# Kernel optimization log

Measured on AMD Instinct MI355X. Metric: run time of the kernel, lower is better.

Reference implementation:

```python
import jax, jax.numpy as jnp
import numpy as np

B, CIN, COUT, H, W = 4, 256, 256, 64, 64
EPS = 1e-5


def _conv1x1(x, w, b):
    # x: [B,C,H,W], w: [O,C], b: [O]
    return jnp.einsum('bchw,oc->bohw', x, w) + b[:, None, None]


def _conv3x3(x, w, b):
    y = jax.lax.conv_general_dilated(x, w, (1, 1), 'SAME',
                                     dimension_numbers=('NCHW', 'OIHW', 'NCHW'))
    return y + b[:, None, None]


def _bn(x, g, b, m, v):
    # inference-mode BatchNorm2d
    return g[:, None, None] * (x - m[:, None, None]) * jax.lax.rsqrt(v[:, None, None] + EPS) + b[:, None, None]


def setup_inputs():
    key = jax.random.key(0)
    keys = iter(jax.random.split(key, 64))
    nrm = lambda shape, s=0.05: jax.random.normal(next(keys), shape, dtype=jnp.float32) * s
    uni = lambda shape: jax.random.uniform(next(keys), shape, dtype=jnp.float32, minval=0.5, maxval=1.5)
    C, C2 = COUT, COUT // 2
    d = {}
    d['x'] = nrm((B, CIN, H, W), 1.0)
    d['wq'] = nrm((C2, CIN)); d['bq'] = nrm((C2,))
    d['wk'] = nrm((C2, CIN)); d['bk'] = nrm((C2,))
    d['wv'] = nrm((C, CIN)); d['bv'] = nrm((C,))
    d['d1_w'] = nrm((C, C)); d['d1_b'] = nrm((C,))
    for p in ['bn1', 'lbn1', 'lbn2', 'lbn3']:
        d[p + '_g'] = uni((C,)); d[p + '_b'] = nrm((C,))
        d[p + '_m'] = nrm((C,)); d[p + '_v'] = uni((C,))
    d['l1_w'] = nrm((C, C)); d['l1_b'] = nrm((C,))
    d['l2_w'] = nrm((C, C, 3, 3)); d['l2_b'] = nrm((C,))
    d['l3_w'] = nrm((C, C)); d['l3_b'] = nrm((C,))
    d['r1_w'] = nrm((C2, C)); d['r1_b'] = nrm((C2,))
    d['rbn_g'] = uni((C2,)); d['rbn_b'] = nrm((C2,))
    d['rbn_m'] = nrm((C2,)); d['rbn_v'] = uni((C2,))
    d['r2_w'] = nrm((C, C2)); d['r2_b'] = nrm((C,))
    return d


def _forward(x, wq, bq, wk, bk, wv, bv, d1_w, d1_b,
             bn1_g, bn1_b, bn1_m, bn1_v,
             l1_w, l1_b, lbn1_g, lbn1_b, lbn1_m, lbn1_v,
             l2_w, l2_b, lbn2_g, lbn2_b, lbn2_m, lbn2_v,
             l3_w, l3_b, lbn3_g, lbn3_b, lbn3_m, lbn3_v,
             r1_w, r1_b, rbn_g, rbn_b, rbn_m, rbn_v, r2_w, r2_b):
    b, _, h, w = x.shape
    n = h * w
    q = _conv1x1(x, wq, bq).reshape(b, -1, n)   # [B, C/2, N]
    k = _conv1x1(x, wk, bk).reshape(b, -1, n)   # [B, C/2, N]
    v = _conv1x1(x, wv, bv).reshape(b, -1, n)   # [B, C,   N]
    energy = jnp.einsum('bcn,bcm->bnm', q, k)   # [B, N, N] (query^T key)
    attn = jax.nn.softmax(energy, axis=-1)
    # feature = bmm(value, attn^T): feat[b,c,n] = sum_m v[b,c,m] * attn[b,n,m]
    feat = jnp.einsum('bcm,bnm->bcn', v, attn).reshape(b, -1, h, w)
    # dual1 gate: sigmoid(relu(bn(conv1x1(feat))))
    gate1 = jax.nn.sigmoid(jax.nn.relu(_bn(_conv1x1(feat, d1_w, d1_b), bn1_g, bn1_b, bn1_m, bn1_v)))
    y = feat * gate1
    # dual2_l: 1x1 -> 3x3 -> 1x1 conv/bn/relu stack
    yl = jax.nn.relu(_bn(_conv1x1(y, l1_w, l1_b), lbn1_g, lbn1_b, lbn1_m, lbn1_v))
    yl = jax.nn.relu(_bn(_conv3x3(yl, l2_w, l2_b), lbn2_g, lbn2_b, lbn2_m, lbn2_v))
    yl = jax.nn.relu(_bn(_conv1x1(yl, l3_w, l3_b), lbn3_g, lbn3_b, lbn3_m, lbn3_v))
    # dual2_r: global-avg-pool SE branch
    pooled = jnp.mean(y, axis=(2, 3), keepdims=True)  # [B, C, 1, 1]
    yr = jax.nn.relu(_bn(_conv1x1(pooled, r1_w, r1_b), rbn_g, rbn_b, rbn_m, rbn_v))
    yr = _conv1x1(yr, r2_w, r2_b)
    return feat * jax.nn.sigmoid(yl + yr)


def reference(x, wq, bq, wk, bk, wv, bv, d1_w, d1_b,
              bn1_g, bn1_b, bn1_m, bn1_v,
              l1_w, l1_b, lbn1_g, lbn1_b, lbn1_m, lbn1_v,
              l2_w, l2_b, lbn2_g, lbn2_b, lbn2_m, lbn2_v,
              l3_w, l3_b, lbn3_g, lbn3_b, lbn3_m, lbn3_v,
              r1_w, r1_b, rbn_g, rbn_b, rbn_m, rbn_v, r2_w, r2_b):
    return _forward(x, wq, bq, wk, bk, wv, bv, d1_w, d1_b,
                    bn1_g, bn1_b, bn1_m, bn1_v,
                    l1_w, l1_b, lbn1_g, lbn1_b, lbn1_m, lbn1_v,
                    l2_w, l2_b, lbn2_g, lbn2_b, lbn2_m, lbn2_v,
                    l3_w, l3_b, lbn3_g, lbn3_b, lbn3_m, lbn3_v,
                    r1_w, r1_b, rbn_g, rbn_b, rbn_m, rbn_v, r2_w, r2_b)
```

## Files before the change

kernel.cpp:

```cpp
#include <hip/hip_runtime.h>
#include <math.h>

#define NPIX 4096
#define EPSBN 1e-5f

typedef __attribute__((ext_vector_type(8))) short bf16x8;
typedef __attribute__((ext_vector_type(4))) float f32x4;

__device__ __forceinline__ float sigmoidf_(float x) { return 1.0f / (1.0f + expf(-x)); }

__device__ __forceinline__ short f2bf(float f) {
    unsigned u = __float_as_uint(f);
    u += 0x7fffu + ((u >> 16) & 1u);
    return (short)(u >> 16);
}
__device__ __forceinline__ float bf2f(short s) {
    return __uint_as_float(((unsigned)(unsigned short)s) << 16);
}
__device__ __forceinline__ int pk2(float lo, float hi) {
    return (int)(unsigned short)f2bf(lo) | ((int)(unsigned short)f2bf(hi) << 16);
}

__device__ __forceinline__ void gl_lds16(const short* g, short* l) {
    __builtin_amdgcn_global_load_lds(
        (const __attribute__((address_space(1))) void*)g,
        (__attribute__((address_space(3))) void*)l, 16, 0, 0);
}

template <int EPI, int BM, int BN>
__global__ __launch_bounds__(256) void gbt_k(
    const short* __restrict__ A, int lda,
    const short* __restrict__ B, int ldb,
    void* __restrict__ Cv, void* __restrict__ Cv2, int Ktot,
    const float* __restrict__ bias, const float* __restrict__ bias2,
    const float* __restrict__ bng, const float* __restrict__ bnb,
    const float* __restrict__ bnm, const float* __restrict__ bnv,
    const short* __restrict__ aux, const float* __restrict__ yrp)
{
    constexpr int FI = BM / 32, FJ = BN / 32;
    constexpr int SA = BM / 64, SB = BN / 64;
    __shared__ alignas(16) short lsA[2 * BM * 32];
    __shared__ alignas(16) short lsB[2 * BN * 32];

    const int tid = threadIdx.x;
    const int l = tid & 63;
    const int wv = tid >> 6;
    const int wm = wv >> 1, wn = wv & 1;
    const int m0 = blockIdx.y * BM;
    const int n0 = blockIdx.x * BN;

    const short* arow[2];
    const short* brow[2];
#pragma unroll
    for (int s = 0; s < SA; ++s) {
        int r = wv * (16 * SA) + s * 16 + (l >> 2);
        int sd = (l & 3) ^ ((r >> 1) & 3);
        if (EPI == 5) {
            int g = m0 + r;
            int p = (g >> 12) * 4356 + (((g & 4095) >> 6) + 1) * 66 + ((g & 63) + 1);
            arow[s] = A + (size_t)p * 256 + (sd << 3);
        } else {
            arow[s] = A + (size_t)(m0 + r) * lda + (sd << 3);
        }
    }
#pragma unroll
    for (int s = 0; s < SB; ++s) {
        int r = wv * (16 * SB) + s * 16 + (l >> 2);
        int sd = (l & 3) ^ ((r >> 1) & 3);
        brow[s] = B + (size_t)(n0 + r) * ldb + (sd << 3);
    }

    const int ks = l >> 4;
    const int lc = l & 15;
    int aoff[FI], boff[FJ];
#pragma unroll
    for (int f = 0; f < FI; ++f) {
        int ra = wm * (BM / 2) + f * 16 + lc;
        aoff[f] = ra * 64 + ((ks ^ ((ra >> 1) & 3)) << 4);
    }
#pragma unroll
    for (int f = 0; f < FJ; ++f) {
        int rb = wn * (BN / 2) + f * 16 + lc;
        boff[f] = rb * 64 + ((ks ^ ((rb >> 1) & 3)) << 4);
    }

    auto stage = [&](int d, int k0l) {
        int eA, eB;
        if (EPI == 5) {
            int t = k0l >> 8, ci0 = k0l & 255;
            eA = ((t / 3) * 66 + (t % 3) - 67) * 256 + ci0;
            eB = t * 65536 + ci0;
        } else {
            eA = k0l; eB = k0l;
        }
        short* dA = lsA + d * (BM * 32) + wv * (SA * 512);
        short* dB = lsB + d * (BN * 32) + wv * (SB * 512);
#pragma unroll
        for (int s = 0; s < SA; ++s) gl_lds16(arow[s] + eA, dA + s * 512);
#pragma unroll
        for (int s = 0; s < SB; ++s) gl_lds16(brow[s] + eB, dB + s * 512);
    };

    f32x4 acc[FI][FJ] = {};
    const int nt = Ktot >> 5;

    stage(0, 0);
    __syncthreads();
    int cur = 0;
    for (int t = 0; t < nt; ++t) {
        if (t + 1 < nt) stage(cur ^ 1, (t + 1) << 5);
        bf16x8 af[FI], bfr[FJ];
#pragma unroll
        for (int f = 0; f < FI; ++f)
            af[f] = *(const bf16x8*)((const char*)lsA + cur * (BM * 64) + aoff[f]);
#pragma unroll
        for (int f = 0; f < FJ; ++f)
            bfr[f] = *(const bf16x8*)((const char*)lsB + cur * (BN * 64) + boff[f]);
#pragma unroll
        for (int i = 0; i < FI; ++i)
#pragma unroll
            for (int j = 0; j < FJ; ++j)
                acc[i][j] = __builtin_amdgcn_mfma_f32_16x16x32_bf16(af[i], bfr[j], acc[i][j], 0, 0, 0);
        __syncthreads();
        cur ^= 1;
    }

    const int lr = (l >> 4) << 2;
#pragma unroll
    for (int i = 0; i < FI; ++i) {
        const int rowl = wm * (BM / 2) + i * 16 + lr;
#pragma unroll
        for (int j = 0; j < FJ; ++j) {
            const int coll = n0 + wn * (BN / 2) + j * 16 + lc;

            float sc = 0.f, tc = 0.f, bi = 0.f;
            if constexpr (EPI == 1) {
                bi = (coll < 128) ? bias[coll] : bias2[coll - 128];
            } else if constexpr (EPI == 3 || EPI == 4 || EPI == 5) {
                sc = bng[coll] * rsqrtf(bnv[coll] + EPSBN);
                tc = bnb[coll] - bnm[coll] * sc;
                bi = bias[coll];
            }

#pragma unroll
            for (int r = 0; r < 4; ++r) {
                const int row = m0 + rowl + r;
                float vvv = acc[i][j][r];
                if constexpr (EPI == 1) {
                    float val = vvv + bi;
                    short hi = f2bf(val);
                    short lo = f2bf(val - bf2f(hi));
                    size_t rb = (size_t)row * 256;
                    if (coll < 128) {
                        short* qb_ = (short*)Cv;
                        qb_[rb + coll] = hi;
                        qb_[rb + 128 + coll] = lo;
                    } else {
                        short* kb_ = (short*)Cv2;
                        int c = coll - 128;
                        kb_[rb + c] = hi;
                        kb_[rb + 128 + c] = lo;
                    }
                } else if constexpr (EPI == 2) {
                    int bb = coll >> 12;
                    ((short*)Cv)[((size_t)bb * 256 + row) * 4096 + (coll & 4095)] = f2bf(vvv + bias[row]);
                } else if constexpr (EPI == 3) {
                    float g = sigmoidf_(fmaxf(sc * (vvv + bi) + tc, 0.f));
                    float fv = bf2f(aux[(size_t)row * 256 + coll]);
                    ((short*)Cv)[(size_t)row * 256 + coll] = f2bf(fv * g);
                } else if constexpr (EPI == 4) {
                    float rv = fmaxf(sc * (vvv + bi) + tc, 0.f);
                    int bb = row >> 12, n = row & 4095;
                    int pr = bb * 4356 + ((n >> 6) + 1) * 66 + (n & 63) + 1;
                    ((short*)Cv)[(size_t)pr * 256 + coll] = f2bf(rv);
                } else if constexpr (EPI == 5) {
                    float rv = fmaxf(sc * (vvv + bi) + tc, 0.f);
                    ((short*)Cv)[(size_t)row * 256 + coll] = f2bf(rv);
                } else if constexpr (EPI == 6) {
                    float s6 = bng[row] * rsqrtf(bnv[row] + EPSBN);
                    float t6 = bnb[row] - bnm[row] * s6;
                    int bb = coll >> 12;
                    float yl = fmaxf(s6 * (vvv + bias[row]) + t6, 0.f);
                    float sg = sigmoidf_(yl + yrp[bb * 256 + row]);
                    float fv = bf2f(aux[(size_t)coll * 256 + row]);
                    ((float*)Cv)[((size_t)bb * 256 + row) * 4096 + (coll & 4095)] = fv * sg;
                }
            }
        }
    }
}

__global__ __launch_bounds__(512, 2) void flash_k(
    const short* __restrict__ Q, const short* __restrict__ K,
    const short* __restrict__ V, short* __restrict__ Op, float* __restrict__ lp)
{
    __shared__ alignas(16) short smem[32768];

    const int tid = threadIdx.x;
    const int l = tid & 63;
    const int wv = tid >> 6;
    const int bid = blockIdx.x;
    const int combo = bid & 15;
    const int batch = combo >> 2;
    const int kvq = combo & 3;
    const int q0 = (bid >> 4) * 256;
    const int kv0 = kvq * 1024;

    const short* Qb = Q + (size_t)batch * 4096 * 256;
    const short* Kb = K + (size_t)batch * 4096 * 256;
    const short* Vb = V + (size_t)batch * 256 * 4096;

    const int lc = l & 15, ks = l >> 4;

    bf16x8 bq[2][8];
#pragma unroll
    for (int f = 0; f < 2; ++f)
#pragma unroll
        for (int cc = 0; cc < 8; ++cc)
            bq[f][cc] = *(const bf16x8*)(Qb +
                (size_t)(q0 + wv * 32 + f * 16 + lc) * 256 + cc * 32 + ks * 8);

    const short* ksrc[2]; short* kdst[2];
    const short* vsrc[2]; short* vdst[2];
#pragma unroll
    for (int i = 0; i < 2; ++i) {
        int row = wv * 4 + i * 2 + (l >> 5);
        int s = l & 31;
        int g = s ^ (row & 7);
        ksrc[i] = Kb + (size_t)(kv0 + row) * 256 + g * 8;
        kdst[i] = smem + wv * 1024 + i * 512;
        int c = wv * 32 + i * 16 + (l >> 2);
        int sv = l & 3;
        int gv = sv ^ ((c >> 1) & 3);
        vsrc[i] = Vb + (size_t)c * 4096 + kv0 + gv * 8;
        vdst[i] = smem + 16384 + wv * 1024 + i * 512;
    }
    auto stageKV = [&](int buf, int t) {
#pragma unroll
        for (int i = 0; i < 2; ++i) gl_lds16(ksrc[i] + (size_t)t * 8192, kdst[i] + buf * 8192);
#pragma unroll
        for (int i = 0; i < 2; ++i) gl_lds16(vsrc[i] + t * 32, vdst[i] + buf * 8192);
    };

    stageKV(0, 0);
    __syncthreads();

    const int kro = lc * 512;
    const int kxr = lc & 7;
    const int vb0 = lc * 64 + ((ks ^ ((lc >> 1) & 3)) << 4);
    const int addrA = (((ks & 1) * 2) * 16 + lc) * 4;
    const int addrB = addrA + 64;

    bf16x8 ones;
#pragma unroll
    for (int e = 0; e < 8; ++e) ones[e] = (short)0x3F80;

    f32x4 acc_o[2][16] = {};
    f32x4 acc_l[2] = {};

    int cur = 0;
    for (int t = 0; t < 32; ++t) {
        if (t + 1 < 32) stageKV(cur ^ 1, t + 1);

        const char* kb_ = (const char*)smem + cur * 16384;
        f32x4 s00 = {}, s01 = {}, s10 = {}, s11 = {};
        __builtin_amdgcn_s_setprio(1);
#pragma unroll
        for (int jc = 0; jc < 4; ++jc) {
#pragma unroll
            for (int kvf = 0; kvf < 2; ++kvf) {
                const char* rb_ = kb_ + kro + kvf * 8192;
                bf16x8 kh_ = *(const bf16x8*)(rb_ + ((((jc * 4) + ks) ^ kxr) << 4));
                bf16x8 kl_ = *(const bf16x8*)(rb_ + (((((jc + 4) * 4) + ks) ^ kxr) << 4));
                f32x4& sA = kvf ? s01 : s00;
                f32x4& sB = kvf ? s11 : s10;
                sA = __builtin_amdgcn_mfma_f32_16x16x32_bf16(kh_, bq[0][jc], sA, 0, 0, 0);
                sB = __builtin_amdgcn_mfma_f32_16x16x32_bf16(kh_, bq[1][jc], sB, 0, 0, 0);
                sA = __builtin_amdgcn_mfma_f32_16x16x32_bf16(kl_, bq[0][jc], sA, 0, 0, 0);
                sB = __builtin_amdgcn_mfma_f32_16x16x32_bf16(kl_, bq[1][jc], sB, 0, 0, 0);
                sA = __builtin_amdgcn_mfma_f32_16x16x32_bf16(kh_, bq[0][jc + 4], sA, 0, 0, 0);
                sB = __builtin_amdgcn_mfma_f32_16x16x32_bf16(kh_, bq[1][jc + 4], sB, 0, 0, 0);
            }
        }
        __builtin_amdgcn_s_setprio(0);

        bf16x8 pa[2];
#pragma unroll
        for (int f = 0; f < 2; ++f) {
            const f32x4& sa = f ? s10 : s00;
            const f32x4& sb = f ? s11 : s01;
            int u0 = pk2(__expf(sa[0]), __expf(sa[1]));
            int u1 = pk2(__expf(sa[2]), __expf(sa[3]));
            int u2 = pk2(__expf(sb[0]), __expf(sb[1]));
            int u3 = pk2(__expf(sb[2]), __expf(sb[3]));
            int a0 = __builtin_amdgcn_ds_bpermute(addrA, u0);
            int b0 = __builtin_amdgcn_ds_bpermute(addrA, u2);
            int a1 = __builtin_amdgcn_ds_bpermute(addrA, u1);
            int b1 = __builtin_amdgcn_ds_bpermute(addrA, u3);
            int a2 = __builtin_amdgcn_ds_bpermute(addrB, u0);
            int b2 = __builtin_amdgcn_ds_bpermute(addrB, u2);
            int a3 = __builtin_amdgcn_ds_bpermute(addrB, u1);
            int b3 = __builtin_amdgcn_ds_bpermute(addrB, u3);
            union { int i4[4]; bf16x8 v; } un;
            un.i4[0] = (ks < 2) ? a0 : b0;
            un.i4[1] = (ks < 2) ? a1 : b1;
            un.i4[2] = (ks < 2) ? a2 : b2;
            un.i4[3] = (ks < 2) ? a3 : b3;
            pa[f] = un.v;
        }

        const char* vbb = (const char*)smem + 32768 + cur * 16384;
        __builtin_amdgcn_s_setprio(1);
#pragma unroll
        for (int j = 0; j < 16; ++j) {
            bf16x8 vv = *(const bf16x8*)(vbb + vb0 + j * 1024);
            acc_o[0][j] = __builtin_amdgcn_mfma_f32_16x16x32_bf16(pa[0], vv, acc_o[0][j], 0, 0, 0);
            acc_o[1][j] = __builtin_amdgcn_mfma_f32_16x16x32_bf16(pa[1], vv, acc_o[1][j], 0, 0, 0);
        }
        acc_l[0] = __builtin_amdgcn_mfma_f32_16x16x32_bf16(pa[0], ones, acc_l[0], 0, 0, 0);
        acc_l[1] = __builtin_amdgcn_mfma_f32_16x16x32_bf16(pa[1], ones, acc_l[1], 0, 0, 0);
        __builtin_amdgcn_s_setprio(0);
        __syncthreads();
        cur ^= 1;
    }

    short* Ob = Op + ((size_t)combo * 4096 + q0 + wv * 32) * 256;
#pragma unroll
    for (int f = 0; f < 2; ++f)
#pragma unroll
        for (int j = 0; j < 16; ++j)
#pragma unroll
            for (int r = 0; r < 4; ++r)
                Ob[(size_t)(f * 16 + ks * 4 + r) * 256 + j * 16 + lc] = f2bf(acc_o[f][j][r]);
    if (lc == 0) {
        float* lb = lp + (size_t)combo * 4096 + q0 + wv * 32;
#pragma unroll
        for (int f = 0; f < 2; ++f)
#pragma unroll
            for (int r = 0; r < 4; ++r)
                lb[f * 16 + ks * 4 + r] = acc_l[f][r];
    }
}

__global__ __launch_bounds__(256) void combine_k(const short* __restrict__ Op,
                                                 const float* __restrict__ lp,
                                                 short* __restrict__ o)
{
    int idx = blockIdx.x * 256 + threadIdx.x;
    size_t e = (size_t)idx * 4;
    int row = (int)(e >> 8);
    int batch = row >> 12, ql = row & 4095;
    int c = (int)(e & 255);
    size_t lbase = (size_t)batch * 4 * 4096 + ql;
    float li = 1.0f / (lp[lbase] + lp[lbase + 4096] + lp[lbase + 8192] + lp[lbase + 12288]);
    size_t base = ((size_t)(batch * 4) * 4096 + ql) * 256 + c;
    const short4 a = *(const short4*)(Op + base);
    const short4 b = *(const short4*)(Op + base + 1048576);
    const short4 cc = *(const short4*)(Op + base + 2097152);
    const short4 d = *(const short4*)(Op + base + 3145728);
    short4 o4;
    o4.x = f2bf((bf2f(a.x) + bf2f(b.x) + bf2f(cc.x) + bf2f(d.x)) * li);
    o4.y = f2bf((bf2f(a.y) + bf2f(b.y) + bf2f(cc.y) + bf2f(d.y)) * li);
    o4.z = f2bf((bf2f(a.z) + bf2f(b.z) + bf2f(cc.z) + bf2f(d.z)) * li);
    o4.w = f2bf((bf2f(a.w) + bf2f(b.w) + bf2f(cc.w) + bf2f(d.w)) * li);
    *(short4*)(o + (size_t)row * 256 + c) = o4;
}

__global__ __launch_bounds__(256) void transpose_x_k(const float* __restrict__ x,
                                                     short* __restrict__ xT3)
{
    __shared__ float t[64][65];
    const int b = blockIdx.z, c0 = blockIdx.y * 64, n0 = blockIdx.x * 64;
    const int tid = threadIdx.x;
#pragma unroll
    for (int rep = 0; rep < 16; ++rep) {
        int idx = tid + rep * 256;
        int i = idx >> 6, j = idx & 63;
        t[i][j] = x[((size_t)(b * 256 + c0 + i)) * NPIX + n0 + j];
    }
    __syncthreads();
#pragma unroll
    for (int rep = 0; rep < 16; ++rep) {
        int idx = tid + rep * 256;
        int i = idx >> 6, j = idx & 63;
        float v = t[j][i];
        short hi = f2bf(v);
        short lo = f2bf(v - bf2f(hi));
        size_t rb = ((size_t)(b * NPIX + n0 + i)) * 768;
        xT3[rb + c0 + j] = hi;
        xT3[rb + 256 + c0 + j] = hi;
        xT3[rb + 512 + c0 + j] = lo;
    }
}

__global__ __launch_bounds__(256) void prep_k(
    const float* __restrict__ wq, const float* __restrict__ wk,
    const float* __restrict__ wvp, const float* __restrict__ d1w,
    const float* __restrict__ l1w, const float* __restrict__ l3w,
    const float* __restrict__ l2w,
    short* __restrict__ wqk3, short* __restrict__ wvb, short* __restrict__ d1wb,
    short* __restrict__ l1wb, short* __restrict__ l3wb, short* __restrict__ w2b)
{
    const int b = blockIdx.x;
    const int tid = threadIdx.x;
    if (b < 256) {
        int idx = b * 256 + tid;
        int o = idx >> 8, c = idx & 255;
        const float* src = (o < 128) ? wq : wk;
        float v = src[(o & 127) * 256 + c];
        short hi = f2bf(v);
        short lo = f2bf(v - bf2f(hi));
        size_t rb = (size_t)o * 768;
        wqk3[rb + c] = hi;
        wqk3[rb + 256 + c] = lo;
        wqk3[rb + 512 + c] = hi;
    } else if (b < 1280) {
        int g = (b - 256) >> 8;
        int i = ((b - 256) & 255) * 256 + tid;
        const float* s = g == 0 ? wvp : g == 1 ? d1w : g == 2 ? l1w : l3w;
        short* d = g == 0 ? wvb : g == 1 ? d1wb : g == 2 ? l1wb : l3wb;
        d[i] = f2bf(s[i]);
    } else {
        int idx = (b - 1280) * 256 + tid;
        int t = idx >> 16;
        int rem = idx & 65535;
        int co = rem >> 8, ci = rem & 255;
        w2b[idx] = f2bf(l2w[((size_t)(co * 256 + ci)) * 9 + t]);
    }
}

__global__ __launch_bounds__(256) void pool_s1_k(const short* __restrict__ yT,
                                                 float* __restrict__ ppart)
{
    const int ns = blockIdx.x, cg = blockIdx.y, b = blockIdx.z;
    const int tid = threadIdx.x;
    const int cl = tid & 63, ph = tid >> 6;
    float s = 0.f;
    const int nbase = ns * 256;
    for (int n = ph; n < 256; n += 4)
        s += bf2f(yT[((size_t)(b * NPIX + nbase + n)) * 256 + cg * 64 + cl]);
    __shared__ float ls[4][64];
    ls[ph][cl] = s;
    __syncthreads();
    if (ph == 0)
        ppart[((size_t)(b * 4 + cg) * 16 + ns) * 64 + cl] =
            ls[0][cl] + ls[1][cl] + ls[2][cl] + ls[3][cl];
}

__global__ __launch_bounds__(256) void pool_s2_k(const float* __restrict__ ppart,
                                                 float* __restrict__ pooled)
{
    const int b = blockIdx.x;
    const int c = threadIdx.x;
    const int cg = c >> 6, cl = c & 63;
    float s = 0.f;
#pragma unroll
    for (int ns = 0; ns < 16; ++ns)
        s += ppart[((size_t)(b * 4 + cg) * 16 + ns) * 64 + cl];
    pooled[b * 256 + c] = s * (1.0f / NPIX);
}

__global__ __launch_bounds__(256) void se_k(
    const float* __restrict__ pooled,
    const float* __restrict__ r1w, const float* __restrict__ r1b,
    const float* __restrict__ g, const float* __restrict__ bb,
    const float* __restrict__ m, const float* __restrict__ vv,
    const float* __restrict__ r2w, const float* __restrict__ r2b,
    float* __restrict__ yr)
{
    const int b = blockIdx.x;
    const int tid = threadIdx.x;
    __shared__ float p[256], hbuf[128];
    p[tid] = pooled[b * 256 + tid];
    __syncthreads();
    if (tid < 128) {
        float a = r1b[tid];
        for (int ci = 0; ci < 256; ++ci) a = fmaf(r1w[tid * 256 + ci], p[ci], a);
        float s = g[tid] * rsqrtf(vv[tid] + EPSBN);
        float t = bb[tid] - m[tid] * s;
        hbuf[tid] = fmaxf(s * a + t, 0.f);
    }
    __syncthreads();
    float a = r2b[tid];
    for (int c2 = 0; c2 < 128; ++c2) a = fmaf(r2w[tid * 128 + c2], hbuf[c2], a);
    yr[b * 256 + tid] = a;
}

extern "C" void kernel_launch(void* const* d_in, const int* in_sizes, int n_in,
                              void* d_out, int out_size, void* d_ws, size_t ws_size,
                              hipStream_t stream)
{
    const float* x    = (const float*)d_in[0];
    const float* wq   = (const float*)d_in[1];
    const float* bq   = (const float*)d_in[2];
    const float* wk   = (const float*)d_in[3];
    const float* bk   = (const float*)d_in[4];
    const float* wvp  = (const float*)d_in[5];
    const float* bv   = (const float*)d_in[6];
    const float* d1w  = (const float*)d_in[7];
    const float* d1b  = (const float*)d_in[8];
    const float* bn1g = (const float*)d_in[9];
    const float* bn1b = (const float*)d_in[10];
    const float* bn1m = (const float*)d_in[11];
    const float* bn1v = (const float*)d_in[12];
    const float* lbn1g = (const float*)d_in[13];
    const float* lbn1b = (const float*)d_in[14];
    const float* lbn1m = (const float*)d_in[15];
    const float* lbn1v = (const float*)d_in[16];
    const float* lbn2g = (const float*)d_in[17];
    const float* lbn2b = (const float*)d_in[18];
    const float* lbn2m = (const float*)d_in[19];
    const float* lbn2v = (const float*)d_in[20];
    const float* lbn3g = (const float*)d_in[21];
    const float* lbn3b = (const float*)d_in[22];
    const float* lbn3m = (const float*)d_in[23];
    const float* lbn3v = (const float*)d_in[24];
    const float* l1w  = (const float*)d_in[25];
    const float* l1b  = (const float*)d_in[26];
    const float* l2w  = (const float*)d_in[27];
    const float* l2b  = (const float*)d_in[28];
    const float* l3w  = (const float*)d_in[29];
    const float* l3b  = (const float*)d_in[30];
    const float* r1w  = (const float*)d_in[31];
    const float* r1b  = (const float*)d_in[32];
    const float* rbng = (const float*)d_in[33];
    const float* rbnb = (const float*)d_in[34];
    const float* rbnm = (const float*)d_in[35];
    const float* rbnv = (const float*)d_in[36];
    const float* r2w  = (const float*)d_in[37];
    const float* r2b  = (const float*)d_in[38];

    float* out = (float*)d_out;
    char* wsb = (char*)d_ws;

    short* xT3  = (short*)(wsb);
    short* qbuf = (short*)(wsb + (24ull << 20));
    short* kbuf = (short*)(wsb + (32ull << 20));
    short* vbuf = (short*)(wsb + (40ull << 20));
    short* Opart= (short*)(wsb + (48ull << 20));
    short* featT= (short*)(wsb + (112ull << 20));
    float* lpart= (float*)(wsb + (120ull << 20));
    short* yT   = (short*)(wsb + (48ull << 20));
    short* t1pad= (short*)(wsb + (56ull << 20));
    short* t2T  = (short*)(wsb + (65ull << 20));
    short* wqk3 = (short*)(wsb + (121ull << 20));
    short* wvb  = wqk3 + 196608;
    short* d1wb = wvb + 65536;
    short* l1wb = d1wb + 65536;
    short* l3wb = l1wb + 65536;
    short* w2b  = l3wb + 65536;
    float* pooled = (float*)(wsb + (123ull << 20) + (512ull << 10));
    float* yrb  = pooled + 1024;
    float* ppart= yrb + 1024;

    dim3 blk(256);

    transpose_x_k<<<dim3(64, 4, 4), blk, 0, stream>>>(x, xT3);
    prep_k<<<3584, blk, 0, stream>>>(wq, wk, wvp, d1w, l1w, l3w, l2w,
                                     wqk3, wvb, d1wb, l1wb, l3wb, w2b);

    gbt_k<1, 128, 64><<<dim3(4, 128), blk, 0, stream>>>(xT3, 768, wqk3, 768, qbuf, kbuf, 768,
        bq, bk, nullptr, nullptr, nullptr, nullptr, nullptr, nullptr);
    gbt_k<2, 64, 128><<<dim3(128, 4), blk, 0, stream>>>(wvb, 256, xT3, 768, vbuf, nullptr, 256,
        bv, nullptr, nullptr, nullptr, nullptr, nullptr, nullptr, nullptr);

    flash_k<<<256, dim3(512), 0, stream>>>(qbuf, kbuf, vbuf, Opart, lpart);
    combine_k<<<4096, blk, 0, stream>>>(Opart, lpart, featT);

    gbt_k<3, 128, 64><<<dim3(4, 128), blk, 0, stream>>>(featT, 256, d1wb, 256, yT, nullptr, 256,
        d1b, nullptr, bn1g, bn1b, bn1m, bn1v, featT, nullptr);

    hipMemsetAsync(t1pad, 0, (size_t)4 * 4356 * 256 * 2, stream);

    pool_s1_k<<<dim3(16, 4, 4), blk, 0, stream>>>(yT, ppart);
    pool_s2_k<<<4, blk, 0, stream>>>(ppart, pooled);
    se_k<<<4, blk, 0, stream>>>(pooled, r1w, r1b, rbng, rbnb, rbnm, rbnv, r2w, r2b, yrb);

    gbt_k<4, 128, 64><<<dim3(4, 128), blk, 0, stream>>>(yT, 256, l1wb, 256, t1pad, nullptr, 256,
        l1b, nullptr, lbn1g, lbn1b, lbn1m, lbn1v, nullptr, nullptr);
    gbt_k<5, 128, 64><<<dim3(4, 128), blk, 0, stream>>>(t1pad, 256, w2b, 256, t2T, nullptr, 2304,
        l2b, nullptr, lbn2g, lbn2b, lbn2m, lbn2v, nullptr, nullptr);

    gbt_k<6, 64, 128><<<dim3(128, 4), blk, 0, stream>>>(l3wb, 256, t2T, 256, out, nullptr, 256,
        l3b, nullptr, lbn3g, lbn3b, lbn3m, lbn3v, featT, yrb);
}
```

Before: 250.5 us.

## Fuse pooling into gate GEMM, shrink split x buffer, drop bpermute in flash

Three separate changes. The channel-sum for global average pooling is now fused into the EPI==3 GEMM epilogue, which writes per-block partial sums, so the pool_s1 pass that re-read yT is removed. The x hi/lo split buffer shrinks from three copies to two, and the QK GEMM reuses the hi half through an index remap, which cuts the transpose write traffic. In flash attention, K rows are loaded into LDS in a permuted order, so the exp'd probabilities can be packed straight into the MFMA operand without ds_bpermute shuffles. The risk is correctness of the row permutation and the extra __syncthreads in the epilogue.

```diff
diff --git a/kernel.cpp b/kernel.cpp
--- a/kernel.cpp
+++ b/kernel.cpp
@@ -90,6 +90,9 @@
             int t = k0l >> 8, ci0 = k0l & 255;
             eA = ((t / 3) * 66 + (t % 3) - 67) * 256 + ci0;
             eB = t * 65536 + ci0;
+        } else if (EPI == 1) {
+            eA = (k0l < 256) ? k0l : k0l - 256;
+            eB = k0l;
         } else {
             eA = k0l; eB = k0l;
         }
@@ -125,6 +128,7 @@
         cur ^= 1;
     }
 
+    float colsum[FJ < 1 ? 1 : FJ] = {};
     const int lr = (l >> 4) << 2;
 #pragma unroll
     for (int i = 0; i < FI; ++i) {
@@ -167,7 +171,9 @@
                 } else if constexpr (EPI == 3) {
                     float g = sigmoidf_(fmaxf(sc * (vvv + bi) + tc, 0.f));
                     float fv = bf2f(aux[(size_t)row * 256 + coll]);
-                    ((short*)Cv)[(size_t)row * 256 + coll] = f2bf(fv * g);
+                    float yv = fv * g;
+                    ((short*)Cv)[(size_t)row * 256 + coll] = f2bf(yv);
+                    colsum[j] += yv;
                 } else if constexpr (EPI == 4) {
                     float rv = fmaxf(sc * (vvv + bi) + tc, 0.f);
                     int bb = row >> 12, n = row & 4095;
@@ -188,6 +194,22 @@
             }
         }
     }
+
+    if constexpr (EPI == 3) {
+        float* lsum = (float*)lsA;
+#pragma unroll
+        for (int j = 0; j < FJ; ++j) {
+            int cl = wn * (BN / 2) + j * 16 + lc;
+            lsum[cl * 8 + wm * 4 + ks] = colsum[j];
+        }
+        __syncthreads();
+        if (tid < BN) {
+            float s = 0.f;
+#pragma unroll
+            for (int u = 0; u < 8; ++u) s += lsum[tid * 8 + u];
+            ((float*)Cv2)[(size_t)blockIdx.y * 256 + n0 + tid] = s;
+        }
+    }
 }
 
 __global__ __launch_bounds__(512, 2) void flash_k(
@@ -224,10 +246,11 @@
     const short* vsrc[2]; short* vdst[2];
 #pragma unroll
     for (int i = 0; i < 2; ++i) {
-        int row = wv * 4 + i * 2 + (l >> 5);
+        int slot = wv * 4 + i * 2 + (l >> 5);
+        int grow = ((slot >> 2) & 3) * 8 + (slot >> 4) * 4 + (slot & 3);
         int s = l & 31;
-        int g = s ^ (row & 7);
-        ksrc[i] = Kb + (size_t)(kv0 + row) * 256 + g * 8;
+        int g = s ^ (slot & 7);
+        ksrc[i] = Kb + (size_t)(kv0 + grow) * 256 + g * 8;
         kdst[i] = smem + wv * 1024 + i * 512;
         int c = wv * 32 + i * 16 + (l >> 2);
         int sv = l & 3;
@@ -248,8 +271,6 @@
     const int kro = lc * 512;
     const int kxr = lc & 7;
     const int vb0 = lc * 64 + ((ks ^ ((lc >> 1) & 3)) << 4);
-    const int addrA = (((ks & 1) * 2) * 16 + lc) * 4;
-    const int addrB = addrA + 64;
 
     bf16x8 ones;
 #pragma unroll
@@ -289,23 +310,11 @@
         for (int f = 0; f < 2; ++f) {
             const f32x4& sa = f ? s10 : s00;
             const f32x4& sb = f ? s11 : s01;
-            int u0 = pk2(__expf(sa[0]), __expf(sa[1]));
-            int u1 = pk2(__expf(sa[2]), __expf(sa[3]));
-            int u2 = pk2(__expf(sb[0]), __expf(sb[1]));
-            int u3 = pk2(__expf(sb[2]), __expf(sb[3]));
-            int a0 = __builtin_amdgcn_ds_bpermute(addrA, u0);
-            int b0 = __builtin_amdgcn_ds_bpermute(addrA, u2);
-            int a1 = __builtin_amdgcn_ds_bpermute(addrA, u1);
-            int b1 = __builtin_amdgcn_ds_bpermute(addrA, u3);
-            int a2 = __builtin_amdgcn_ds_bpermute(addrB, u0);
-            int b2 = __builtin_amdgcn_ds_bpermute(addrB, u2);
-            int a3 = __builtin_amdgcn_ds_bpermute(addrB, u1);
-            int b3 = __builtin_amdgcn_ds_bpermute(addrB, u3);
             union { int i4[4]; bf16x8 v; } un;
-            un.i4[0] = (ks < 2) ? a0 : b0;
-            un.i4[1] = (ks < 2) ? a1 : b1;
-            un.i4[2] = (ks < 2) ? a2 : b2;
-            un.i4[3] = (ks < 2) ? a3 : b3;
+            un.i4[0] = pk2(__expf(sa[0]), __expf(sa[1]));
+            un.i4[1] = pk2(__expf(sa[2]), __expf(sa[3]));
+            un.i4[2] = pk2(__expf(sb[0]), __expf(sb[1]));
+            un.i4[3] = pk2(__expf(sb[2]), __expf(sb[3]));
             pa[f] = un.v;
         }
 
@@ -367,7 +376,7 @@
 }
 
 __global__ __launch_bounds__(256) void transpose_x_k(const float* __restrict__ x,
-                                                     short* __restrict__ xT3)
+                                                     short* __restrict__ xT2)
 {
     __shared__ float t[64][65];
     const int b = blockIdx.z, c0 = blockIdx.y * 64, n0 = blockIdx.x * 64;
@@ -386,10 +395,9 @@
         float v = t[j][i];
         short hi = f2bf(v);
         short lo = f2bf(v - bf2f(hi));
-        size_t rb = ((size_t)(b * NPIX + n0 + i)) * 768;
-        xT3[rb + c0 + j] = hi;
-        xT3[rb + 256 + c0 + j] = hi;
-        xT3[rb + 512 + c0 + j] = lo;
+        size_t rb = ((size_t)(b * NPIX + n0 + i)) * 512;
+        xT2[rb + c0 + j] = hi;
+        xT2[rb + 256 + c0 + j] = lo;
     }
 }
 
@@ -429,34 +437,15 @@
     }
 }
 
-__global__ __launch_bounds__(256) void pool_s1_k(const short* __restrict__ yT,
-                                                 float* __restrict__ ppart)
-{
-    const int ns = blockIdx.x, cg = blockIdx.y, b = blockIdx.z;
-    const int tid = threadIdx.x;
-    const int cl = tid & 63, ph = tid >> 6;
-    float s = 0.f;
-    const int nbase = ns * 256;
-    for (int n = ph; n < 256; n += 4)
-        s += bf2f(yT[((size_t)(b * NPIX + nbase + n)) * 256 + cg * 64 + cl]);
-    __shared__ float ls[4][64];
-    ls[ph][cl] = s;
-    __syncthreads();
-    if (ph == 0)
-        ppart[((size_t)(b * 4 + cg) * 16 + ns) * 64 + cl] =
-            ls[0][cl] + ls[1][cl] + ls[2][cl] + ls[3][cl];
-}
-
-__global__ __launch_bounds__(256) void pool_s2_k(const float* __restrict__ ppart,
+__global__ __launch_bounds__(256) void pool_s2_k(const float* __restrict__ pp2,
                                                  float* __restrict__ pooled)
 {
     const int b = blockIdx.x;
     const int c = threadIdx.x;
-    const int cg = c >> 6, cl = c & 63;
     float s = 0.f;
 #pragma unroll
-    for (int ns = 0; ns < 16; ++ns)
-        s += ppart[((size_t)(b * 4 + cg) * 16 + ns) * 64 + cl];
+    for (int k = 0; k < 32; ++k)
+        s += pp2[(size_t)(b * 32 + k) * 256 + c];
     pooled[b * 256 + c] = s * (1.0f / NPIX);
 }
 
@@ -533,7 +522,7 @@
     float* out = (float*)d_out;
     char* wsb = (char*)d_ws;
 
-    short* xT3  = (short*)(wsb);
+    short* xT2  = (short*)(wsb);
     short* qbuf = (short*)(wsb + (24ull << 20));
     short* kbuf = (short*)(wsb + (32ull << 20));
     short* vbuf = (short*)(wsb + (40ull << 20));
@@ -551,29 +540,28 @@
     short* w2b  = l3wb + 65536;
     float* pooled = (float*)(wsb + (123ull << 20) + (512ull << 10));
     float* yrb  = pooled + 1024;
-    float* ppart= yrb + 1024;
+    float* ppart2 = yrb + 1024;
 
     dim3 blk(256);
 
-    transpose_x_k<<<dim3(64, 4, 4), blk, 0, stream>>>(x, xT3);
+    transpose_x_k<<<dim3(64, 4, 4), blk, 0, stream>>>(x, xT2);
     prep_k<<<3584, blk, 0, stream>>>(wq, wk, wvp, d1w, l1w, l3w, l2w,
                                      wqk3, wvb, d1wb, l1wb, l3wb, w2b);
 
-    gbt_k<1, 128, 64><<<dim3(4, 128), blk, 0, stream>>>(xT3, 768, wqk3, 768, qbuf, kbuf, 768,
+    gbt_k<1, 128, 64><<<dim3(4, 128), blk, 0, stream>>>(xT2, 512, wqk3, 768, qbuf, kbuf, 768,
         bq, bk, nullptr, nullptr, nullptr, nullptr, nullptr, nullptr);
-    gbt_k<2, 64, 128><<<dim3(128, 4), blk, 0, stream>>>(wvb, 256, xT3, 768, vbuf, nullptr, 256,
+    gbt_k<2, 64, 128><<<dim3(128, 4), blk, 0, stream>>>(wvb, 256, xT2, 512, vbuf, nullptr, 256,
         bv, nullptr, nullptr, nullptr, nullptr, nullptr, nullptr, nullptr);
 
     flash_k<<<256, dim3(512), 0, stream>>>(qbuf, kbuf, vbuf, Opart, lpart);
     combine_k<<<4096, blk, 0, stream>>>(Opart, lpart, featT);
 
-    gbt_k<3, 128, 64><<<dim3(4, 128), blk, 0, stream>>>(featT, 256, d1wb, 256, yT, nullptr, 256,
+    gbt_k<3, 128, 64><<<dim3(4, 128), blk, 0, stream>>>(featT, 256, d1wb, 256, yT, ppart2, 256,
         d1b, nullptr, bn1g, bn1b, bn1m, bn1v, featT, nullptr);
 
     hipMemsetAsync(t1pad, 0, (size_t)4 * 4356 * 256 * 2, stream);
 
-    pool_s1_k<<<dim3(16, 4, 4), blk, 0, stream>>>(yT, ppart);
-    pool_s2_k<<<4, blk, 0, stream>>>(ppart, pooled);
+    pool_s2_k<<<4, blk, 0, stream>>>(ppart2, pooled);
     se_k<<<4, blk, 0, stream>>>(pooled, r1w, r1b, rbng, rbnb, rbnm, rbnv, r2w, r2b, yrb);
 
     gbt_k<4, 128, 64><<<dim3(4, 128), blk, 0, stream>>>(yT, 256, l1wb, 256, t1pad, nullptr, 256,
```

Result: faster. 224.6 us (-10.3%).
